# Kernel tuning notes

Hardware: AMD Instinct MI355X
Metric: run time of the kernel (lower is better)

Reference implementation:

```python
import jax, jax.numpy as jnp
import numpy as np

B, D, H, O = 8192, 512, 16384, 1000

def _row_normalize(w):
    return w / jnp.linalg.norm(w, axis=1, keepdims=True)

def setup_inputs() -> dict:
    key = jax.random.key(0)
    k0, k1, k2, k3 = jax.random.split(key, 4)
    x = jax.random.normal(k0, (B, D), dtype=jnp.float32)
    kohonen_weights = _row_normalize(jax.random.normal(k1, (H, D), dtype=jnp.float32))
    G_fwd = _row_normalize(jax.random.normal(k2, (O, H), dtype=jnp.float32))
    G_rev = _row_normalize(jax.random.normal(k3, (D, H), dtype=jnp.float32))
    return {"x": x, "kohonen_weights": kohonen_weights, "G_fwd": G_fwd, "G_rev": G_rev}

def reference(x, kohonen_weights, G_fwd, G_rev):
    # torch.cdist(x, W): Euclidean distances, shape (B, H).
    x2 = jnp.sum(x * x, axis=1, keepdims=True)          # (B, 1)
    w2 = jnp.sum(kohonen_weights * kohonen_weights, axis=1)  # (H,)
    d2 = x2 - 2.0 * (x @ kohonen_weights.T) + w2[None, :]    # (B, H)
    distances = jnp.sqrt(jnp.maximum(d2, 0.0))
    winners = jnp.argmin(distances, axis=1)              # (B,)
    # one_hot @ G_fwd.T == gather of G_fwd columns (same math, no dense GEMM)
    output = G_fwd.T[winners]                            # (B, O)
    recos = G_rev.T[winners]                             # (B, D)
    return (output, recos, winners)
```

## Files before the change

### kernel.cpp

```cpp
#include <hip/hip_runtime.h>
#include <stdint.h>

constexpr int kB = 8192;
constexpr int kD = 512;
constexpr int kH = 16384;
constexpr int kO = 1000;
constexpr int kNB64 = kH / 64;
constexpr float kMargin = 0.04f;

typedef _Float16 half8v __attribute__((ext_vector_type(8)));
typedef _Float16 half4v __attribute__((ext_vector_type(4)));
typedef float float4v __attribute__((ext_vector_type(4)));

#define VMW(n) asm volatile("s_waitcnt vmcnt(" #n ")" ::: "memory")

constexpr size_t OFF_XH  = 0;
constexpr size_t OFF_WH  = OFF_XH + (size_t)kB * kD * 2;
constexpr size_t OFF_W2  = OFF_WH + (size_t)kH * kD * 2;
constexpr size_t OFF_BT  = OFF_W2 + 65536;
constexpr size_t OFF_GFT = OFF_BT + (size_t)kB * kNB64 * 16;
constexpr size_t OFF_GRT = OFF_GFT + (size_t)kH * kO * 4;
constexpr size_t WS_NEED = OFF_GRT + (size_t)kH * kD * 4;

__device__ inline unsigned long long packkey(float s, int h) {
    unsigned u = __float_as_uint(s);
    u ^= (u & 0x80000000u) ? 0xFFFFFFFFu : 0x80000000u;
    return ((unsigned long long)u << 32) | (unsigned)h;
}
__device__ inline float unpacks(unsigned long long k) {
    unsigned u = (unsigned)(k >> 32);
    u ^= (u & 0x80000000u) ? 0x80000000u : 0xFFFFFFFFu;
    return __uint_as_float(u);
}
__device__ inline unsigned long long shfl_xor_u64(unsigned long long v, int m) {
    unsigned lo = (unsigned)v, hi = (unsigned)(v >> 32);
    lo = __shfl_xor(lo, m, 64);
    hi = __shfl_xor(hi, m, 64);
    return ((unsigned long long)hi << 32) | lo;
}
__device__ inline unsigned long long u64min(unsigned long long a, unsigned long long b) {
    return a < b ? a : b;
}

template <typename T>
__device__ inline void gload_lds16(const T* g, T* l) {
    __builtin_amdgcn_global_load_lds(
        (const __attribute__((address_space(1))) uint32_t*)g,
        (__attribute__((address_space(3))) uint32_t*)l, 16, 0, 0);
}

__global__ __launch_bounds__(256) void prep_kernel(const float* __restrict__ x,
                                                   const float* __restrict__ W,
                                                   _Float16* __restrict__ xh,
                                                   _Float16* __restrict__ wh,
                                                   float* __restrict__ w2) {
    if (blockIdx.x < 2048) {
        size_t i = (size_t)blockIdx.x * 256 + threadIdx.x;
        const float4* s4 = reinterpret_cast<const float4*>(x);
        float4 a = s4[i * 2], b = s4[i * 2 + 1];
        half8v h = {(_Float16)a.x, (_Float16)a.y, (_Float16)a.z, (_Float16)a.w,
                    (_Float16)b.x, (_Float16)b.y, (_Float16)b.z, (_Float16)b.w};
        *reinterpret_cast<half8v*>(xh + i * 8) = h;
    } else {
        int bx = blockIdx.x - 2048;
        int lane = threadIdx.x & 63;
        int wv   = threadIdx.x >> 6;
        int row  = bx * 4 + wv;
        const float4* Wr = reinterpret_cast<const float4*>(W + (size_t)row * kD);
        float s = 0.f;
#pragma unroll
        for (int i = 0; i < 2; ++i) {
            float4 v = Wr[lane + i * 64];
            s += v.x * v.x + v.y * v.y + v.z * v.z + v.w * v.w;
            half4v h = {(_Float16)v.x, (_Float16)v.y, (_Float16)v.z, (_Float16)v.w};
            *reinterpret_cast<half4v*>(wh + (size_t)row * kD + i * 256 + lane * 4) = h;
        }
#pragma unroll
        for (int off = 32; off; off >>= 1) s += __shfl_xor(s, off, 64);
        if (lane == 0) w2[row] = s;
    }
}

__global__ __launch_bounds__(256) void transpose2_kernel(const float* __restrict__ Gf,
                                                         float* __restrict__ GfT,
                                                         const float* __restrict__ Gr,
                                                         float* __restrict__ GrT,
                                                         int useTf, int useTr) {
    const float* src; float* dst; int R, r0;
    if (blockIdx.y < 32) {
        if (!useTf) return;
        src = Gf; dst = GfT; R = kO; r0 = blockIdx.y * 32;
    } else {
        if (!useTr) return;
        src = Gr; dst = GrT; R = kD; r0 = (blockIdx.y - 32) * 32;
    }
    const int C = kH;
    __shared__ float s[32][33];
    const int tx = threadIdx.x & 31;
    const int ty = threadIdx.x >> 5;
    const int c0 = blockIdx.x * 32;
#pragma unroll
    for (int i = 0; i < 4; ++i) {
        int r = r0 + ty + i * 8;
        if (r < R) s[ty + i * 8][tx] = src[(size_t)r * C + c0 + tx];
    }
    __syncthreads();
#pragma unroll
    for (int i = 0; i < 4; ++i) {
        int c = c0 + ty + i * 8;
        if (r0 + tx < R) dst[(size_t)c * R + r0 + tx] = s[tx][ty + i * 8];
    }
}

__global__ __launch_bounds__(512, 2) void gemm_argmin_mfma(
    const _Float16* __restrict__ xh, const _Float16* __restrict__ wh,
    const float* __restrict__ w2, ulonglong2* __restrict__ blocktop)
{
    __shared__ __align__(16) _Float16 sm[65536];

    const int tid  = threadIdx.x;
    const int lane = tid & 63;
    const int wv   = tid >> 6;
    const int wr   = wv >> 2;
    const int wc   = wv & 3;

    int bid = blockIdx.x;
    int swz = (bid & 7) * (2048 / 8) + (bid >> 3);
    const int hb  = swz & 63;
    const int mb  = swz >> 6;
    const int bm0 = mb * 256, hn0 = hb * 256;

    float4v acc[8][4];
#pragma unroll
    for (int i = 0; i < 8; ++i)
#pragma unroll
        for (int j = 0; j < 4; ++j) acc[i][j] = (float4v){0.f, 0.f, 0.f, 0.f};

    auto STAGEH = [&](int h) {
        const int T2 = h >> 2, jp = h & 3;
        const int kk = jp >> 1, isB = jp & 1;
        const int kt = T2 * 64 + kk * 32;
        _Float16* dst0 = &sm[(((T2 & 1) << 2) | jp) * 8192 + wv * 512];
#pragma unroll
        for (int l = 0; l < 2; ++l) {
            const int idx = l * 512 + tid;
            const int r = idx >> 2, c = idx & 3;
            const int sc = c ^ ((r >> 1) & 3);
            const _Float16* src =
                (isB ? wh + (size_t)(hn0 + r) * kD : xh + (size_t)(bm0 + r) * kD)
                + kt + sc * 8;
            gload_lds16(src, dst0 + l * 4096);
        }
    };

    auto PH2 = [&](int buf, int kk, int q) {
        const int fbase = buf * 32768 + kk * 16384;
        half8v bfr[4], afr[8];
#pragma unroll
        for (int jn = 0; jn < 4; ++jn) {
            const int r = wc * 64 + jn * 16 + (lane & 15);
            const int cs = (lane >> 4) ^ ((r >> 1) & 3);
            bfr[jn] = *reinterpret_cast<const half8v*>(&sm[fbase + 8192 + r * 32 + cs * 8]);
        }
#pragma unroll
        for (int im = 0; im < 8; ++im) {
            const int r = wr * 128 + im * 16 + (lane & 15);
            const int cs = (lane >> 4) ^ ((r >> 1) & 3);
            afr[im] = *reinterpret_cast<const half8v*>(&sm[fbase + r * 32 + cs * 8]);
        }
        if (q < 16) {
            const int h = 4 * (q >> 1) + 2 * (q & 1);
            STAGEH(h);
            STAGEH(h + 1);
        }
        __builtin_amdgcn_s_barrier();
        asm volatile("s_waitcnt lgkmcnt(0)" ::: "memory");
        __builtin_amdgcn_sched_barrier(0);
        __builtin_amdgcn_s_setprio(1);
#pragma unroll
        for (int im = 0; im < 8; ++im)
#pragma unroll
            for (int jn = 0; jn < 4; ++jn)
                acc[im][jn] =
                    __builtin_amdgcn_mfma_f32_16x16x32_f16(afr[im], bfr[jn],
                                                           acc[im][jn], 0, 0, 0);
        __builtin_amdgcn_s_setprio(0);
    };

    STAGEH(0); STAGEH(1);
    STAGEH(2); STAGEH(3);
    STAGEH(4); STAGEH(5);
    VMW(8);
    __builtin_amdgcn_s_barrier();

    PH2(0, 0, 3);  VMW(8); __builtin_amdgcn_s_barrier();
    PH2(0, 1, 4);  VMW(8); __builtin_amdgcn_s_barrier();
    PH2(1, 0, 5);  VMW(8); __builtin_amdgcn_s_barrier();
    PH2(1, 1, 6);  VMW(8); __builtin_amdgcn_s_barrier();
    PH2(0, 0, 7);  VMW(8); __builtin_amdgcn_s_barrier();
    PH2(0, 1, 8);  VMW(8); __builtin_amdgcn_s_barrier();
    PH2(1, 0, 9);  VMW(8); __builtin_amdgcn_s_barrier();
    PH2(1, 1, 10); VMW(8); __builtin_amdgcn_s_barrier();
    PH2(0, 0, 11); VMW(8); __builtin_amdgcn_s_barrier();
    PH2(0, 1, 12); VMW(8); __builtin_amdgcn_s_barrier();
    PH2(1, 0, 13); VMW(8); __builtin_amdgcn_s_barrier();
    PH2(1, 1, 14); VMW(8); __builtin_amdgcn_s_barrier();
    PH2(0, 0, 15); VMW(8); __builtin_amdgcn_s_barrier();
    PH2(0, 1, 16); VMW(4); __builtin_amdgcn_s_barrier();
    PH2(1, 0, 16); VMW(0); __builtin_amdgcn_s_barrier();
    PH2(1, 1, 16);

    float w2v[4];
#pragma unroll
    for (int j = 0; j < 4; ++j) w2v[j] = w2[hn0 + wc * 64 + j * 16 + (lane & 15)];

#pragma unroll
    for (int i = 0; i < 8; ++i) {
#pragma unroll
        for (int r = 0; r < 4; ++r) {
            unsigned long long k1 = ~0ull, k2 = ~0ull;
#pragma unroll
            for (int j = 0; j < 4; ++j) {
                float s = fmaf(-2.f, acc[i][j][r], w2v[j]);
                unsigned long long key = packkey(s, hn0 + wc * 64 + j * 16 + (lane & 15));
                if (key < k1) { k2 = k1; k1 = key; }
                else if (key < k2) { k2 = key; }
            }
#pragma unroll
            for (int m = 1; m < 16; m <<= 1) {
                unsigned long long o1 = shfl_xor_u64(k1, m);
                unsigned long long o2 = shfl_xor_u64(k2, m);
                unsigned long long n1 = u64min(k1, o1);
                unsigned long long mx = k1 < o1 ? o1 : k1;
                unsigned long long mn = u64min(k2, o2);
                k1 = n1;
                k2 = u64min(mx, mn);
            }
            if ((lane & 15) == 0) {
                int rl = wr * 128 + i * 16 + (lane >> 4) * 4 + r;
                blocktop[(size_t)(bm0 + rl) * kNB64 + hb * 4 + wc] = (ulonglong2){k1, k2};
            }
        }
    }
}

__global__ __launch_bounds__(256) void finish_kernel(
    const float* __restrict__ x, const float* __restrict__ W,
    const float* __restrict__ w2, const ulonglong2* __restrict__ blocktop,
    const float* __restrict__ Gf, const float* __restrict__ Gr,
    const float* __restrict__ GfT, const float* __restrict__ GrT,
    int useTf, int useTr, float* __restrict__ out)
{
    const int tid = threadIdx.x;
    const int b = blockIdx.x;
    __shared__ float xs[kD];
    __shared__ unsigned long long red[256];
    __shared__ unsigned long long sv1, sv2;
    __shared__ int clist[kNB64];
    __shared__ int ccount;

    if (tid < 128)
        reinterpret_cast<float4*>(xs)[tid] =
            reinterpret_cast<const float4*>(x + (size_t)b * kD)[tid];
    if (tid == 0) ccount = 0;

    ulonglong2 t12 = blocktop[(size_t)b * kNB64 + tid];

    red[tid] = t12.x;
    __syncthreads();
    for (int s = 128; s > 0; s >>= 1) {
        if (tid < s) red[tid] = u64min(red[tid], red[tid + s]);
        __syncthreads();
    }
    if (tid == 0) sv1 = red[0];
    __syncthreads();
    const unsigned long long v1k = sv1;
    const float v1s = unpacks(v1k);
    const int b1hb = ((int)(unsigned)(v1k & 0xFFFFFFFFu)) >> 6;

    red[tid] = (tid == b1hb) ? t12.y : t12.x;
    __syncthreads();
    for (int s = 128; s > 0; s >>= 1) {
        if (tid < s) red[tid] = u64min(red[tid], red[tid + s]);
        __syncthreads();
    }
    if (tid == 0) sv2 = red[0];
    __syncthreads();
    const float v2s = unpacks(sv2);

    int idx;
    if (v2s - v1s > kMargin) {
        idx = (int)(unsigned)(v1k & 0xFFFFFFFFu);
    } else {
        if (unpacks(t12.x) <= v1s + kMargin) {
            int p = atomicAdd(&ccount, 1);
            clist[p] = tid;
        }
        __syncthreads();
        const int nc = ccount;
        const int wvf = tid >> 6, lnf = tid & 63;
        unsigned long long bestk = ~0ull;
        for (int c = wvf; c < nc; c += 4) {
            int h = clist[c] * 64 + lnf;
            const float4* wr = reinterpret_cast<const float4*>(W + (size_t)h * kD);
            float dot = 0.f;
            for (int k = 0; k < kD / 4; ++k) {
                float4 wvv = wr[k];
                dot = fmaf(xs[k * 4 + 0], wvv.x, dot);
                dot = fmaf(xs[k * 4 + 1], wvv.y, dot);
                dot = fmaf(xs[k * 4 + 2], wvv.z, dot);
                dot = fmaf(xs[k * 4 + 3], wvv.w, dot);
            }
            float s = fmaf(-2.f, dot, w2[h]);
            bestk = u64min(bestk, packkey(s, h));
        }
        red[tid] = bestk;
        __syncthreads();
        for (int s = 128; s > 0; s >>= 1) {
            if (tid < s) red[tid] = u64min(red[tid], red[tid + s]);
            __syncthreads();
        }
        idx = (int)(unsigned)(red[0] & 0xFFFFFFFFu);
    }

    float* out0 = out;
    float* out1 = out + (size_t)kB * kO;
    float* outw = out + (size_t)kB * (kO + kD);
    if (useTf) {
        const float4* gfr = reinterpret_cast<const float4*>(GfT + (size_t)idx * kO);
        float4* o0 = reinterpret_cast<float4*>(out0 + (size_t)b * kO);
        for (int o = tid; o < kO / 4; o += 256) o0[o] = gfr[o];
    } else {
        for (int o = tid; o < kO; o += 256)
            out0[(size_t)b * kO + o] = Gf[(size_t)o * kH + idx];
    }
    if (useTr) {
        const float4* grr = reinterpret_cast<const float4*>(GrT + (size_t)idx * kD);
        float4* o1 = reinterpret_cast<float4*>(out1 + (size_t)b * kD);
        if (tid < kD / 4) o1[tid] = grr[tid];
    } else {
        for (int d = tid; d < kD; d += 256)
            out1[(size_t)b * kD + d] = Gr[(size_t)d * kH + idx];
    }
    if (tid == 0) outw[b] = (float)idx;
}

extern "C" void kernel_launch(void* const* d_in, const int* in_sizes, int n_in,
                              void* d_out, int out_size, void* d_ws, size_t ws_size,
                              hipStream_t stream) {
    const float* x  = (const float*)d_in[0];
    const float* W  = (const float*)d_in[1];
    const float* Gf = (const float*)d_in[2];
    const float* Gr = (const float*)d_in[3];
    float* out = (float*)d_out;

    char* ws = (char*)d_ws;
    _Float16* xh = (_Float16*)(ws + OFF_XH);
    _Float16* wh = (_Float16*)(ws + OFF_WH);
    float* w2 = (float*)(ws + OFF_W2);
    ulonglong2* blocktop = (ulonglong2*)(ws + OFF_BT);
    float* GfT = (float*)(ws + OFF_GFT);
    float* GrT = (float*)(ws + OFF_GRT);
    const int useTf = (ws_size >= OFF_GRT) ? 1 : 0;
    const int useTr = (ws_size >= WS_NEED) ? 1 : 0;

    hipLaunchKernelGGL(prep_kernel, dim3(2048 + 4096), dim3(256), 0, stream,
                       x, W, xh, wh, w2);
    if (useTf || useTr)
        hipLaunchKernelGGL(transpose2_kernel, dim3(kH / 32, 48), dim3(256), 0, stream,
                           Gf, GfT, Gr, GrT, useTf, useTr);
    hipLaunchKernelGGL(gemm_argmin_mfma, dim3(2048), dim3(512), 0, stream,
                       xh, wh, w2, blocktop);
    hipLaunchKernelGGL(finish_kernel, dim3(kB), dim3(256), 0, stream,
                       x, W, w2, blocktop, Gf, Gr, GfT, GrT, useTf, useTr, out);
}
```

Before: 379.4 us.

## Pack top-2 keys into 32 bits with quantized scores and relax pipeline waits

```diff
diff --git a/kernel.cpp b/kernel.cpp
--- a/kernel.cpp
+++ b/kernel.cpp
@@ -6,7 +6,7 @@
 constexpr int kH = 16384;
 constexpr int kO = 1000;
 constexpr int kNB64 = kH / 64;
-constexpr float kMargin = 0.04f;
+constexpr float kMargin = 0.055f;
 
 typedef _Float16 half8v __attribute__((ext_vector_type(8)));
 typedef _Float16 half4v __attribute__((ext_vector_type(4)));
@@ -18,25 +18,21 @@
 constexpr size_t OFF_WH  = OFF_XH + (size_t)kB * kD * 2;
 constexpr size_t OFF_W2  = OFF_WH + (size_t)kH * kD * 2;
 constexpr size_t OFF_BT  = OFF_W2 + 65536;
-constexpr size_t OFF_GFT = OFF_BT + (size_t)kB * kNB64 * 16;
+constexpr size_t OFF_GFT = OFF_BT + (size_t)kB * kNB64 * 8;
 constexpr size_t OFF_GRT = OFF_GFT + (size_t)kH * kO * 4;
 constexpr size_t WS_NEED = OFF_GRT + (size_t)kH * kD * 4;
 
-__device__ inline unsigned long long packkey(float s, int h) {
+__device__ inline unsigned mono32(float s) {
     unsigned u = __float_as_uint(s);
-    u ^= (u & 0x80000000u) ? 0xFFFFFFFFu : 0x80000000u;
-    return ((unsigned long long)u << 32) | (unsigned)h;
-}
-__device__ inline float unpacks(unsigned long long k) {
-    unsigned u = (unsigned)(k >> 32);
+    return u ^ ((u & 0x80000000u) ? 0xFFFFFFFFu : 0x80000000u);
+}
+__device__ inline float dq32(unsigned key) {
+    unsigned u = key & 0xFFFFFFC0u;
     u ^= (u & 0x80000000u) ? 0x80000000u : 0xFFFFFFFFu;
     return __uint_as_float(u);
 }
-__device__ inline unsigned long long shfl_xor_u64(unsigned long long v, int m) {
-    unsigned lo = (unsigned)v, hi = (unsigned)(v >> 32);
-    lo = __shfl_xor(lo, m, 64);
-    hi = __shfl_xor(hi, m, 64);
-    return ((unsigned long long)hi << 32) | lo;
+__device__ inline unsigned long long packkey(float s, int h) {
+    return ((unsigned long long)mono32(s) << 32) | (unsigned)h;
 }
 __device__ inline unsigned long long u64min(unsigned long long a, unsigned long long b) {
     return a < b ? a : b;
@@ -114,7 +110,7 @@
 
 __global__ __launch_bounds__(512, 2) void gemm_argmin_mfma(
     const _Float16* __restrict__ xh, const _Float16* __restrict__ wh,
-    const float* __restrict__ w2, ulonglong2* __restrict__ blocktop)
+    const float* __restrict__ w2, uint2* __restrict__ blocktop)
 {
     __shared__ __align__(16) _Float16 sm[65536];
 
@@ -190,24 +186,24 @@
     STAGEH(0); STAGEH(1);
     STAGEH(2); STAGEH(3);
     STAGEH(4); STAGEH(5);
-    VMW(8);
+    VMW(4);
     __builtin_amdgcn_s_barrier();
 
-    PH2(0, 0, 3);  VMW(8); __builtin_amdgcn_s_barrier();
-    PH2(0, 1, 4);  VMW(8); __builtin_amdgcn_s_barrier();
-    PH2(1, 0, 5);  VMW(8); __builtin_amdgcn_s_barrier();
-    PH2(1, 1, 6);  VMW(8); __builtin_amdgcn_s_barrier();
-    PH2(0, 0, 7);  VMW(8); __builtin_amdgcn_s_barrier();
-    PH2(0, 1, 8);  VMW(8); __builtin_amdgcn_s_barrier();
-    PH2(1, 0, 9);  VMW(8); __builtin_amdgcn_s_barrier();
-    PH2(1, 1, 10); VMW(8); __builtin_amdgcn_s_barrier();
-    PH2(0, 0, 11); VMW(8); __builtin_amdgcn_s_barrier();
-    PH2(0, 1, 12); VMW(8); __builtin_amdgcn_s_barrier();
-    PH2(1, 0, 13); VMW(8); __builtin_amdgcn_s_barrier();
-    PH2(1, 1, 14); VMW(8); __builtin_amdgcn_s_barrier();
-    PH2(0, 0, 15); VMW(8); __builtin_amdgcn_s_barrier();
-    PH2(0, 1, 16); VMW(4); __builtin_amdgcn_s_barrier();
-    PH2(1, 0, 16); VMW(0); __builtin_amdgcn_s_barrier();
+    PH2(0, 0, 3);           __builtin_amdgcn_s_barrier();
+    PH2(0, 1, 4);  VMW(4);  __builtin_amdgcn_s_barrier();
+    PH2(1, 0, 5);           __builtin_amdgcn_s_barrier();
+    PH2(1, 1, 6);  VMW(4);  __builtin_amdgcn_s_barrier();
+    PH2(0, 0, 7);           __builtin_amdgcn_s_barrier();
+    PH2(0, 1, 8);  VMW(4);  __builtin_amdgcn_s_barrier();
+    PH2(1, 0, 9);           __builtin_amdgcn_s_barrier();
+    PH2(1, 1, 10); VMW(4);  __builtin_amdgcn_s_barrier();
+    PH2(0, 0, 11);          __builtin_amdgcn_s_barrier();
+    PH2(0, 1, 12); VMW(4);  __builtin_amdgcn_s_barrier();
+    PH2(1, 0, 13);          __builtin_amdgcn_s_barrier();
+    PH2(1, 1, 14); VMW(4);  __builtin_amdgcn_s_barrier();
+    PH2(0, 0, 15);          __builtin_amdgcn_s_barrier();
+    PH2(0, 1, 16); VMW(4);  __builtin_amdgcn_s_barrier();
+    PH2(1, 0, 16); VMW(0);  __builtin_amdgcn_s_barrier();
     PH2(1, 1, 16);
 
     float w2v[4];
@@ -218,27 +214,28 @@
     for (int i = 0; i < 8; ++i) {
 #pragma unroll
         for (int r = 0; r < 4; ++r) {
-            unsigned long long k1 = ~0ull, k2 = ~0ull;
+            unsigned k1 = 0xFFFFFFFFu, k2 = 0xFFFFFFFFu;
 #pragma unroll
             for (int j = 0; j < 4; ++j) {
                 float s = fmaf(-2.f, acc[i][j][r], w2v[j]);
-                unsigned long long key = packkey(s, hn0 + wc * 64 + j * 16 + (lane & 15));
+                unsigned key = (mono32(s) & 0xFFFFFFC0u)
+                             | (unsigned)(j * 16 + (lane & 15));
                 if (key < k1) { k2 = k1; k1 = key; }
                 else if (key < k2) { k2 = key; }
             }
 #pragma unroll
             for (int m = 1; m < 16; m <<= 1) {
-                unsigned long long o1 = shfl_xor_u64(k1, m);
-                unsigned long long o2 = shfl_xor_u64(k2, m);
-                unsigned long long n1 = u64min(k1, o1);
-                unsigned long long mx = k1 < o1 ? o1 : k1;
-                unsigned long long mn = u64min(k2, o2);
+                unsigned o1 = (unsigned)__shfl_xor((int)k1, m, 64);
+                unsigned o2 = (unsigned)__shfl_xor((int)k2, m, 64);
+                unsigned n1 = min(k1, o1);
+                unsigned mx = max(k1, o1);
+                k2 = min(min(k2, o2), mx);
                 k1 = n1;
-                k2 = u64min(mx, mn);
             }
             if ((lane & 15) == 0) {
                 int rl = wr * 128 + i * 16 + (lane >> 4) * 4 + r;
-                blocktop[(size_t)(bm0 + rl) * kNB64 + hb * 4 + wc] = (ulonglong2){k1, k2};
+                blocktop[(size_t)(bm0 + rl) * kNB64 + hb * 4 + wc] =
+                    (uint2){k1, k2};
             }
         }
     }
@@ -246,7 +243,7 @@
 
 __global__ __launch_bounds__(256) void finish_kernel(
     const float* __restrict__ x, const float* __restrict__ W,
-    const float* __restrict__ w2, const ulonglong2* __restrict__ blocktop,
+    const float* __restrict__ w2, const uint2* __restrict__ blocktop,
     const float* __restrict__ Gf, const float* __restrict__ Gr,
     const float* __restrict__ GfT, const float* __restrict__ GrT,
     int useTf, int useTr, float* __restrict__ out)
@@ -264,9 +261,9 @@
             reinterpret_cast<const float4*>(x + (size_t)b * kD)[tid];
     if (tid == 0) ccount = 0;
 
-    ulonglong2 t12 = blocktop[(size_t)b * kNB64 + tid];
-
-    red[tid] = t12.x;
+    uint2 t12 = blocktop[(size_t)b * kNB64 + tid];
+
+    red[tid] = ((unsigned long long)t12.x << 8) | (unsigned)tid;
     __syncthreads();
     for (int s = 128; s > 0; s >>= 1) {
         if (tid < s) red[tid] = u64min(red[tid], red[tid + s]);
@@ -275,10 +272,12 @@
     if (tid == 0) sv1 = red[0];
     __syncthreads();
     const unsigned long long v1k = sv1;
-    const float v1s = unpacks(v1k);
-    const int b1hb = ((int)(unsigned)(v1k & 0xFFFFFFFFu)) >> 6;
-
-    red[tid] = (tid == b1hb) ? t12.y : t12.x;
+    const int b1hb = (int)(v1k & 0xFFu);
+    const unsigned v1key = (unsigned)(v1k >> 8);
+    const float v1s = dq32(v1key);
+    const int v1h = b1hb * 64 + (int)(v1key & 63u);
+
+    red[tid] = ((unsigned long long)((tid == b1hb) ? t12.y : t12.x) << 8) | (unsigned)tid;
     __syncthreads();
     for (int s = 128; s > 0; s >>= 1) {
         if (tid < s) red[tid] = u64min(red[tid], red[tid + s]);
@@ -286,13 +285,13 @@
     }
     if (tid == 0) sv2 = red[0];
     __syncthreads();
-    const float v2s = unpacks(sv2);
+    const float v2s = dq32((unsigned)(sv2 >> 8));
 
     int idx;
     if (v2s - v1s > kMargin) {
-        idx = (int)(unsigned)(v1k & 0xFFFFFFFFu);
-    } else {
-        if (unpacks(t12.x) <= v1s + kMargin) {
+        idx = v1h;
+    } else {
+        if (dq32(t12.x) <= v1s + kMargin) {
             int p = atomicAdd(&ccount, 1);
             clist[p] = tid;
         }
@@ -358,7 +357,7 @@
     _Float16* xh = (_Float16*)(ws + OFF_XH);
     _Float16* wh = (_Float16*)(ws + OFF_WH);
     float* w2 = (float*)(ws + OFF_W2);
-    ulonglong2* blocktop = (ulonglong2*)(ws + OFF_BT);
+    uint2* blocktop = (uint2*)(ws + OFF_BT);
     float* GfT = (float*)(ws + OFF_GFT);
     float* GrT = (float*)(ws + OFF_GRT);
     const int useTf = (ws_size >= OFF_GRT) ? 1 : 0;
```

New measurement: 324.8 us. 14.4% less time.
